# Optimization experiments

Hardware: AMD Instinct MI355X
Metric: run time of the kernel (lower is better)

## Reference

```python
import jax, jax.numpy as jnp
import numpy as np

B, N, C_IN, L, C_OUT = 8, 50000, 32, 9, 64
M, NNZ = 12500, 37500


def setup_inputs() -> dict:
    key = jax.random.key(0)
    k = jax.random.split(key, 7)
    x = jax.random.normal(k[0], (B, N, C_IN), dtype=jnp.float32)
    weight = jax.random.normal(k[1], (L * C_IN, C_OUT), dtype=jnp.float32) * (1.0 / np.sqrt(L * C_IN))
    bias = jax.random.normal(k[2], (C_OUT,), dtype=jnp.float32) * 0.01
    values = jax.random.uniform(k[3], (NNZ,), dtype=jnp.float32)
    spiral_indices = jax.random.randint(k[4], (N, L), 0, N, dtype=jnp.int64)
    rows = jax.random.randint(k[5], (NNZ,), 0, M, dtype=jnp.int64)
    cols = jax.random.randint(k[6], (NNZ,), 0, N, dtype=jnp.int64)
    return {"x": x, "weight": weight, "bias": bias, "values": values,
            "spiral_indices": spiral_indices, "rows": rows, "cols": cols,
            "num_out_verts": M}


def reference(x, weight, bias, values, spiral_indices, rows, cols, num_out_verts):
    b, n, c = x.shape
    # SpiralConv: gather spiral neighborhoods, flatten, linear
    g = x[:, spiral_indices]                      # [B, N, L, C]
    g = g.reshape(b, n, -1)                       # [B, N, L*C]
    out = jnp.einsum('bnk,ko->bno', g, weight) + bias
    out = jax.nn.elu(out)                         # [B, N, C_OUT]
    # Pool: sparse down_transform (gather, scale, scatter_add)
    gathered = out[:, cols] * values[None, :, None]          # [B, NNZ, C_OUT]
    pooled = jnp.zeros((b, num_out_verts, out.shape[-1]), dtype=out.dtype)
    pooled = pooled.at[:, rows].add(gathered)                # [B, M, C_OUT]
    return pooled
```

## Files before the change

### kernel.cpp

```cpp
#include <hip/hip_runtime.h>

#define BATCH   8
#define NVERT   50000
#define CIN     32
#define LSP     9
#define COUT    64
#define MVERT   12500
#define NNZ     37500

#define NFRAG   2304
#define OUTDW   (BATCH * MVERT * COUT)

#define TILE_T  128
#define TPB     293

#define PRE_BLOCKS   6250
#define PACK_BLOCKS  9
#define HISTA_BLOCKS 147

#define ROWCAP  96

typedef __attribute__((ext_vector_type(8))) short  short8;
typedef __attribute__((ext_vector_type(4))) float  floatx4;

static __device__ __forceinline__ unsigned short f2bf(float f) {
    union { float f; unsigned int u; } c; c.f = f;
    unsigned int u = c.u;
    return (unsigned short)((u + 0x7fffu + ((u >> 16) & 1u)) >> 16);
}

__global__ __launch_bounds__(256)
void prep_kernel(const float* __restrict__ x, const float* __restrict__ w,
                 const int* __restrict__ rows,
                 unsigned short* __restrict__ x16, unsigned short* __restrict__ wp,
                 int* __restrict__ hist)
{
    const int blk = blockIdx.x;
    const int tid = threadIdx.x;
    if (blk < PRE_BLOCKS) {
        const size_t base = ((size_t)blk * 256 + tid) * 8;
        const float4* s = (const float4*)(x + base);
        float4 a = s[0], c = s[1];
        unsigned short t[8];
        t[0]=f2bf(a.x); t[1]=f2bf(a.y); t[2]=f2bf(a.z); t[3]=f2bf(a.w);
        t[4]=f2bf(c.x); t[5]=f2bf(c.y); t[6]=f2bf(c.z); t[7]=f2bf(c.w);
        *(uint4*)(x16 + base) = *(uint4*)t;
    } else if (blk < PRE_BLOCKS + PACK_BLOCKS) {
        const int f = (blk - PRE_BLOCKS) * 256 + tid;
        if (f < NFRAG) {
            int s = f >> 8, g = (f >> 6) & 3, lane = f & 63;
            int k0 = s * 32 + (lane >> 4) * 8, col = g * 16 + (lane & 15);
            unsigned short t[8];
            #pragma unroll
            for (int j = 0; j < 8; ++j)
                t[j] = f2bf(w[(size_t)(k0 + j) * COUT + col]);
            ((uint4*)wp)[f] = *(uint4*)t;
        }
    } else {
        const int z = (blk - PRE_BLOCKS - PACK_BLOCKS) * 256 + tid;
        if (z < NNZ) atomicAdd(&hist[rows[z]], 1);
    }
}

__global__ __launch_bounds__(1024)
void scan_kernel(const int* __restrict__ hist, int* __restrict__ off2) {
    __shared__ int sh[1024];
    const int t = threadIdx.x;
    const int base = t * 13;
    int loc[13];
    int s = 0;
    #pragma unroll
    for (int j = 0; j < 13; ++j) {
        int i = base + j;
        int v = (i < MVERT) ? hist[i] : 0;
        loc[j] = s; s += v;
    }
    sh[t] = s;
    __syncthreads();
    for (int d = 1; d < 1024; d <<= 1) {
        int v = (t >= d) ? sh[t - d] : 0;
        __syncthreads();
        sh[t] += v;
        __syncthreads();
    }
    const int excl = sh[t] - s;
    #pragma unroll
    for (int j = 0; j < 13; ++j) {
        int i = base + j;
        if (i < MVERT) off2[i] = excl + loc[j];
    }
}

__global__ __launch_bounds__(256)
void scatter_kernel(const int* __restrict__ rows, const int* __restrict__ cols,
                    const float* __restrict__ vals, const int* __restrict__ spiral,
                    int* __restrict__ off2,
                    int* __restrict__ rows_s, float* __restrict__ vals_s,
                    unsigned short* __restrict__ tidx) {
    int z = blockIdx.x * 256 + threadIdx.x;
    if (z < NNZ) {
        int r = rows[z];
        int c = cols[z];
        int pos = atomicAdd(&off2[r], 1);
        rows_s[pos] = r;
        vals_s[pos] = vals[z];
        unsigned short t[16];
        #pragma unroll
        for (int s = 0; s < 9; ++s) t[s] = (unsigned short)spiral[c * LSP + s];
        #pragma unroll
        for (int s = 9; s < 16; ++s) t[s] = 0;
        uint4* dst = (uint4*)(tidx + (size_t)pos * 16);
        dst[0] = *(uint4*)t;
        dst[1] = *(uint4*)(t + 8);
    }
}

__global__ __launch_bounds__(256, 3)
void spiral_mfma7_kernel(const unsigned short* __restrict__ x16,
                         const unsigned short* __restrict__ wp,
                         const float* __restrict__ bias,
                         const unsigned short* __restrict__ tidx,
                         const int* __restrict__ rows_s,
                         const float* __restrict__ vals_s,
                         float* __restrict__ out)
{
    __shared__ float redu[ROWCAP * COUT];

    const int bid  = blockIdx.x;
    const int b    = bid & 7;
    const int tile = bid >> 3;
    const int tid  = threadIdx.x;
    const int w    = tid >> 6;
    const int lane = tid & 63;
    const int quad = lane >> 4;
    const int m16  = lane & 15;
    const int z0w  = tile * TILE_T + 32 * w;

    const int z0        = tile * TILE_T;
    const int zl        = min(z0 + TILE_T - 1, NNZ - 1);
    const int first_row = rows_s[z0];
    const int last_row  = rows_s[zl];
    const int span      = last_row - first_row + 1;
    const int lim       = min(span, ROWCAP);

    const int   zc   = min(z0w + (lane & 31), NNZ - 1);
    const int   rowv = rows_s[zc];
    const float valv = vals_s[zc];
    const uint4 p0 = *(const uint4*)(tidx + (size_t)zc * 16);
    const unsigned int p1 = *(const unsigned int*)(tidx + (size_t)zc * 16 + 8);
    int idx[9];
    idx[0] = p0.x & 0xffff;  idx[1] = p0.x >> 16;
    idx[2] = p0.y & 0xffff;  idx[3] = p0.y >> 16;
    idx[4] = p0.z & 0xffff;  idx[5] = p0.z >> 16;
    idx[6] = p0.w & 0xffff;  idx[7] = p0.w >> 16;
    idx[8] = p1 & 0xffff;

    const unsigned short* xb = x16 + (size_t)b * NVERT * CIN;

    short8 A[2][9];
    #pragma unroll
    for (int s = 0; s < 9; ++s) {
        #pragma unroll
        for (int mt = 0; mt < 2; ++mt) {
            int tix = __shfl(idx[s], mt * 16 + m16);
            A[mt][s] = *(const short8*)(xb + (size_t)tix * CIN + quad * 8);
        }
    }

    for (int i = tid; i < lim * COUT; i += 256) redu[i] = 0.0f;
    __syncthreads();

    floatx4 acc[2][4];
    #pragma unroll
    for (int mt = 0; mt < 2; ++mt)
        #pragma unroll
        for (int g = 0; g < 4; ++g) acc[mt][g] = (floatx4){0.f, 0.f, 0.f, 0.f};

    #pragma unroll
    for (int s = 0; s < 9; ++s) {
        short8 bf[4];
        #pragma unroll
        for (int g = 0; g < 4; ++g)
            bf[g] = *(const short8*)(wp + (size_t)((s * 4 + g) * 64 + lane) * 8);
        #pragma unroll
        for (int mt = 0; mt < 2; ++mt)
            #pragma unroll
            for (int g = 0; g < 4; ++g)
                acc[mt][g] = __builtin_amdgcn_mfma_f32_16x16x32_bf16(A[mt][s], bf[g], acc[mt][g], 0, 0, 0);
    }

    float bs[4];
    #pragma unroll
    for (int g = 0; g < 4; ++g) bs[g] = bias[g * 16 + m16];
    float* outb = out + (size_t)b * MVERT * COUT;

    #pragma unroll
    for (int mt = 0; mt < 2; ++mt) {
        int   rr[4]; float vv[4]; bool val[4];
        #pragma unroll
        for (int r = 0; r < 4; ++r) {
            const int tsk = mt * 16 + quad * 4 + r;
            rr[r]  = __shfl(rowv, tsk);
            vv[r]  = __shfl(valv, tsk);
            val[r] = (z0w + tsk) < NNZ;
        }
        bool emit[4];
        #pragma unroll
        for (int r = 0; r < 4; ++r)
            emit[r] = (r == 3) || (!val[r + 1 > 3 ? 3 : r + 1]) || (rr[r + 1 > 3 ? 3 : r + 1] != rr[r]);
        #pragma unroll
        for (int g = 0; g < 4; ++g) {
            const int ch = g * 16 + m16;
            float s = 0.0f;
            #pragma unroll
            for (int r = 0; r < 4; ++r) {
                if (val[r]) {
                    float y = acc[mt][g][r] + bs[g];
                    y = (y > 0.0f) ? y : (__expf(y) - 1.0f);
                    s += y * vv[r];
                    if (emit[r]) {
                        const int local = rr[r] - first_row;
                        if (local < ROWCAP)
                            atomicAdd(&redu[local * COUT + ch], s);
                        else
                            atomicAdd(outb + (size_t)rr[r] * COUT + ch, s);
                        s = 0.0f;
                    }
                }
            }
        }
    }

    __syncthreads();

    for (int i = tid; i < lim * (COUT / 4); i += 256) {
        const int local = i >> 4;
        const int c4    = (i & 15) * 4;
        const int row   = first_row + local;
        const float4 v  = *(const float4*)(redu + local * COUT + c4);
        float* dst = outb + (size_t)row * COUT + c4;
        if (row == first_row || row == last_row) {
            atomicAdd(dst + 0, v.x);
            atomicAdd(dst + 1, v.y);
            atomicAdd(dst + 2, v.z);
            atomicAdd(dst + 3, v.w);
        } else {
            *(float4*)dst = v;
        }
    }
}

extern "C" void kernel_launch(void* const* d_in, const int* in_sizes, int n_in,
                              void* d_out, int out_size, void* d_ws, size_t ws_size,
                              hipStream_t stream) {
    const float* x      = (const float*)d_in[0];
    const float* w      = (const float*)d_in[1];
    const float* bias   = (const float*)d_in[2];
    const float* vals   = (const float*)d_in[3];
    const int*   spiral = (const int*)d_in[4];
    const int*   rows   = (const int*)d_in[5];
    const int*   cols   = (const int*)d_in[6];
    float* out = (float*)d_out;

    char* base = (char*)d_ws;
    unsigned short* wp     = (unsigned short*)(base);
    unsigned short* x16    = (unsigned short*)(base + 36864);
    int*            hist   = (int*)(base + 25636864);
    int*            off2   = (int*)(base + 25686864);
    int*            rows_s = (int*)(base + 25736864);
    float*          vals_s = (float*)(base + 26036896);
    unsigned short* tidx   = (unsigned short*)(base + 26186912);

    hipMemsetAsync(hist, 0, MVERT * sizeof(int), stream);
    hipMemsetAsync(out, 0, (size_t)OUTDW * sizeof(float), stream);

    const int prep_grid = PRE_BLOCKS + PACK_BLOCKS + HISTA_BLOCKS;
    prep_kernel<<<prep_grid, 256, 0, stream>>>(x, w, rows, x16, wp, hist);
    scan_kernel<<<1, 1024, 0, stream>>>(hist, off2);
    scatter_kernel<<<147, 256, 0, stream>>>(rows, cols, vals, spiral, off2,
                                            rows_s, vals_s, tidx);
    spiral_mfma7_kernel<<<BATCH * TPB, 256, 0, stream>>>(x16, wp, bias, tidx,
                                                         rows_s, vals_s, out);
}
```

Before: 205.0 us.

## Halve per-block task tile, drop second MFMA row tile, fuse output zeroing into prep

Each block of the fused spiral-MFMA kernel now handles 64 nonzero tasks instead of 128, one 16-row MFMA tile per wave, with a smaller LDS reduction buffer and a launch bound of 4 blocks per CU. The goal is lower register and LDS pressure for higher occupancy and twice as many blocks to hide gather latency. The output zeroing moves from a separate memset into extra blocks of the prep kernel, saving a launch. The cost is more boundary rows that need global atomics, more per-block overhead, and weight fragments reused across fewer tasks.

```diff
diff --git a/kernel.cpp b/kernel.cpp
--- a/kernel.cpp
+++ b/kernel.cpp
@@ -11,14 +11,15 @@
 #define NFRAG   2304
 #define OUTDW   (BATCH * MVERT * COUT)
 
-#define TILE_T  128
-#define TPB     293
+#define TASKS_PB 64
+#define BLK_B    586
 
 #define PRE_BLOCKS   6250
 #define PACK_BLOCKS  9
+#define ZERO_BLOCKS  6250
 #define HISTA_BLOCKS 147
 
-#define ROWCAP  96
+#define ROWCAP  64
 
 typedef __attribute__((ext_vector_type(8))) short  short8;
 typedef __attribute__((ext_vector_type(4))) float  floatx4;
@@ -33,7 +34,7 @@
 void prep_kernel(const float* __restrict__ x, const float* __restrict__ w,
                  const int* __restrict__ rows,
                  unsigned short* __restrict__ x16, unsigned short* __restrict__ wp,
-                 int* __restrict__ hist)
+                 float* __restrict__ out, int* __restrict__ hist)
 {
     const int blk = blockIdx.x;
     const int tid = threadIdx.x;
@@ -56,8 +57,11 @@
                 t[j] = f2bf(w[(size_t)(k0 + j) * COUT + col]);
             ((uint4*)wp)[f] = *(uint4*)t;
         }
+    } else if (blk < PRE_BLOCKS + PACK_BLOCKS + ZERO_BLOCKS) {
+        const size_t base = ((size_t)(blk - PRE_BLOCKS - PACK_BLOCKS) * 256 + tid) * 4;
+        if (base < OUTDW) *(uint4*)(out + base) = (uint4){0, 0, 0, 0};
     } else {
-        const int z = (blk - PRE_BLOCKS - PACK_BLOCKS) * 256 + tid;
+        const int z = (blk - PRE_BLOCKS - PACK_BLOCKS - ZERO_BLOCKS) * 256 + tid;
         if (z < NNZ) atomicAdd(&hist[rows[z]], 1);
     }
 }
@@ -115,14 +119,14 @@
     }
 }
 
-__global__ __launch_bounds__(256, 3)
-void spiral_mfma7_kernel(const unsigned short* __restrict__ x16,
-                         const unsigned short* __restrict__ wp,
-                         const float* __restrict__ bias,
-                         const unsigned short* __restrict__ tidx,
-                         const int* __restrict__ rows_s,
-                         const float* __restrict__ vals_s,
-                         float* __restrict__ out)
+__global__ __launch_bounds__(256, 4)
+void spiral_mfma11_kernel(const unsigned short* __restrict__ x16,
+                          const unsigned short* __restrict__ wp,
+                          const float* __restrict__ bias,
+                          const unsigned short* __restrict__ tidx,
+                          const int* __restrict__ rows_s,
+                          const float* __restrict__ vals_s,
+                          float* __restrict__ out)
 {
     __shared__ float redu[ROWCAP * COUT];
 
@@ -134,16 +138,19 @@
     const int lane = tid & 63;
     const int quad = lane >> 4;
     const int m16  = lane & 15;
-    const int z0w  = tile * TILE_T + 32 * w;
-
-    const int z0        = tile * TILE_T;
-    const int zl        = min(z0 + TILE_T - 1, NNZ - 1);
+    const int z0w  = tile * TASKS_PB + 16 * w;
+
+    const int z0        = tile * TASKS_PB;
+    const int zl        = min(z0 + TASKS_PB - 1, NNZ - 1);
     const int first_row = rows_s[z0];
     const int last_row  = rows_s[zl];
-    const int span      = last_row - first_row + 1;
-    const int lim       = min(span, ROWCAP);
-
-    const int   zc   = min(z0w + (lane & 31), NNZ - 1);
+    const int lim       = min(last_row - first_row + 1, ROWCAP);
+
+    #pragma unroll
+    for (int i = 0; i < 4; ++i)
+        ((uint4*)redu)[i * 256 + tid] = (uint4){0, 0, 0, 0};
+
+    const int   zc   = min(z0w + m16, NNZ - 1);
     const int   rowv = rows_s[zc];
     const float valv = vals_s[zc];
     const uint4 p0 = *(const uint4*)(tidx + (size_t)zc * 16);
@@ -157,24 +164,18 @@
 
     const unsigned short* xb = x16 + (size_t)b * NVERT * CIN;
 
-    short8 A[2][9];
+    short8 A[9];
     #pragma unroll
     for (int s = 0; s < 9; ++s) {
-        #pragma unroll
-        for (int mt = 0; mt < 2; ++mt) {
-            int tix = __shfl(idx[s], mt * 16 + m16);
-            A[mt][s] = *(const short8*)(xb + (size_t)tix * CIN + quad * 8);
-        }
-    }
-
-    for (int i = tid; i < lim * COUT; i += 256) redu[i] = 0.0f;
+        int tix = __shfl(idx[s], m16);
+        A[s] = *(const short8*)(xb + (size_t)tix * CIN + quad * 8);
+    }
+
     __syncthreads();
 
-    floatx4 acc[2][4];
-    #pragma unroll
-    for (int mt = 0; mt < 2; ++mt)
-        #pragma unroll
-        for (int g = 0; g < 4; ++g) acc[mt][g] = (floatx4){0.f, 0.f, 0.f, 0.f};
+    floatx4 acc[4];
+    #pragma unroll
+    for (int g = 0; g < 4; ++g) acc[g] = (floatx4){0.f, 0.f, 0.f, 0.f};
 
     #pragma unroll
     for (int s = 0; s < 9; ++s) {
@@ -183,10 +184,8 @@
         for (int g = 0; g < 4; ++g)
             bf[g] = *(const short8*)(wp + (size_t)((s * 4 + g) * 64 + lane) * 8);
         #pragma unroll
-        for (int mt = 0; mt < 2; ++mt)
-            #pragma unroll
-            for (int g = 0; g < 4; ++g)
-                acc[mt][g] = __builtin_amdgcn_mfma_f32_16x16x32_bf16(A[mt][s], bf[g], acc[mt][g], 0, 0, 0);
+        for (int g = 0; g < 4; ++g)
+            acc[g] = __builtin_amdgcn_mfma_f32_16x16x32_bf16(A[s], bf[g], acc[g], 0, 0, 0);
     }
 
     float bs[4];
@@ -194,38 +193,35 @@
     for (int g = 0; g < 4; ++g) bs[g] = bias[g * 16 + m16];
     float* outb = out + (size_t)b * MVERT * COUT;
 
-    #pragma unroll
-    for (int mt = 0; mt < 2; ++mt) {
-        int   rr[4]; float vv[4]; bool val[4];
+    int   rr[4]; float vv[4]; bool val[4];
+    #pragma unroll
+    for (int r = 0; r < 4; ++r) {
+        const int tsk = quad * 4 + r;
+        rr[r]  = __shfl(rowv, tsk);
+        vv[r]  = __shfl(valv, tsk);
+        val[r] = (z0w + tsk) < NNZ;
+    }
+    bool emit[4];
+    #pragma unroll
+    for (int r = 0; r < 4; ++r)
+        emit[r] = (r == 3) || (!val[r + 1 > 3 ? 3 : r + 1]) || (rr[r + 1 > 3 ? 3 : r + 1] != rr[r]);
+    #pragma unroll
+    for (int g = 0; g < 4; ++g) {
+        const int ch = g * 16 + m16;
+        float s = 0.0f;
         #pragma unroll
         for (int r = 0; r < 4; ++r) {
-            const int tsk = mt * 16 + quad * 4 + r;
-            rr[r]  = __shfl(rowv, tsk);
-            vv[r]  = __shfl(valv, tsk);
-            val[r] = (z0w + tsk) < NNZ;
-        }
-        bool emit[4];
-        #pragma unroll
-        for (int r = 0; r < 4; ++r)
-            emit[r] = (r == 3) || (!val[r + 1 > 3 ? 3 : r + 1]) || (rr[r + 1 > 3 ? 3 : r + 1] != rr[r]);
-        #pragma unroll
-        for (int g = 0; g < 4; ++g) {
-            const int ch = g * 16 + m16;
-            float s = 0.0f;
-            #pragma unroll
-            for (int r = 0; r < 4; ++r) {
-                if (val[r]) {
-                    float y = acc[mt][g][r] + bs[g];
-                    y = (y > 0.0f) ? y : (__expf(y) - 1.0f);
-                    s += y * vv[r];
-                    if (emit[r]) {
-                        const int local = rr[r] - first_row;
-                        if (local < ROWCAP)
-                            atomicAdd(&redu[local * COUT + ch], s);
-                        else
-                            atomicAdd(outb + (size_t)rr[r] * COUT + ch, s);
-                        s = 0.0f;
-                    }
+            if (val[r]) {
+                float y = acc[g][r] + bs[g];
+                y = (y > 0.0f) ? y : (__expf(y) - 1.0f);
+                s += y * vv[r];
+                if (emit[r]) {
+                    const int local = rr[r] - first_row;
+                    if (local < ROWCAP)
+                        atomicAdd(&redu[local * COUT + ch], s);
+                    else
+                        atomicAdd(outb + (size_t)rr[r] * COUT + ch, s);
+                    s = 0.0f;
                 }
             }
         }
@@ -272,13 +268,12 @@
     unsigned short* tidx   = (unsigned short*)(base + 26186912);
 
     hipMemsetAsync(hist, 0, MVERT * sizeof(int), stream);
-    hipMemsetAsync(out, 0, (size_t)OUTDW * sizeof(float), stream);
-
-    const int prep_grid = PRE_BLOCKS + PACK_BLOCKS + HISTA_BLOCKS;
-    prep_kernel<<<prep_grid, 256, 0, stream>>>(x, w, rows, x16, wp, hist);
+
+    const int prep_grid = PRE_BLOCKS + PACK_BLOCKS + ZERO_BLOCKS + HISTA_BLOCKS;
+    prep_kernel<<<prep_grid, 256, 0, stream>>>(x, w, rows, x16, wp, out, hist);
     scan_kernel<<<1, 1024, 0, stream>>>(hist, off2);
     scatter_kernel<<<147, 256, 0, stream>>>(rows, cols, vals, spiral, off2,
                                             rows_s, vals_s, tidx);
-    spiral_mfma7_kernel<<<BATCH * TPB, 256, 0, stream>>>(x16, wp, bias, tidx,
-                                                         rows_s, vals_s, out);
-}
+    spiral_mfma11_kernel<<<BATCH * BLK_B, 256, 0, stream>>>(x16, wp, bias, tidx,
+                                                            rows_s, vals_s, out);
+}
```

After: 204.3 us. No clear change (-0.3%).
